# Performance work log

Hardware: AMD Instinct MI355X
Metric: run time of the kernel (lower is better)

The kernel has to match this reference:

```python
import jax, jax.numpy as jnp
import numpy as np

T, D, H, V, Z = 32, 128, 256, 32000, 256


def _gru_cell(x, h, W_ih, W_hh, b_ih, b_hh):
    # PyTorch GRU cell, gate order r,z,n. x,h: [D,H]
    gi = x @ W_ih.T + b_ih
    gh = h @ W_hh.T + b_hh
    i_r, i_z, i_n = jnp.split(gi, 3, axis=-1)
    h_r, h_z, h_n = jnp.split(gh, 3, axis=-1)
    r = jax.nn.sigmoid(i_r + h_r)
    z = jax.nn.sigmoid(i_z + h_z)
    n = jnp.tanh(i_n + r * h_n)
    return (1.0 - z) * n + z * h


def _tree_rnn(nodes, edges, h0, emb, pc, ps):
    # nodes/edges: [T,D]; h0: [D,H]. Child vs sibling GRU chosen per-node by edges.
    def step(h, te):
        tok, e = te
        x = emb[tok]                       # [D,H]
        hc = _gru_cell(x, h, *pc)
        hs = _gru_cell(x, h, *ps)
        hn = jnp.where(e[:, None], hc, hs)  # branch-aware state update
        return hn, hn                       # seq_len=1, L=1 => output == new state
    h_final, outs = jax.lax.scan(step, h0, (nodes, edges))
    return outs, h_final                    # outs: [T,D,H]


def setup_inputs() -> dict:
    key = jax.random.key(0)
    ks = iter(jax.random.split(key, 48))
    s = 0.05
    def gru():
        return (jax.random.normal(next(ks), (3 * H, H), jnp.float32) * s,
                jax.random.normal(next(ks), (3 * H, H), jnp.float32) * s,
                jnp.zeros((3 * H,), jnp.float32),
                jnp.zeros((3 * H,), jnp.float32))
    inp = {}
    inp['nodes'] = jax.random.randint(next(ks), (T, D), 0, V, dtype=jnp.int32)
    inp['edges'] = jax.random.bernoulli(next(ks), 0.5, (T, D))
    inp['emb'] = jax.random.normal(next(ks), (V, H), jnp.float32) * s
    (inp['enc_c_Wih'], inp['enc_c_Whh'], inp['enc_c_bih'], inp['enc_c_bhh']) = gru()
    (inp['enc_s_Wih'], inp['enc_s_Whh'], inp['enc_s_bih'], inp['enc_s_bhh']) = gru()
    (inp['dec_c_Wih'], inp['dec_c_Whh'], inp['dec_c_bih'], inp['dec_c_bhh']) = gru()
    (inp['dec_s_Wih'], inp['dec_s_Whh'], inp['dec_s_bih'], inp['dec_s_bhh']) = gru()
    inp['W_mean'] = jax.random.normal(next(ks), (Z, H), jnp.float32) * s
    inp['b_mean'] = jnp.zeros((Z,), jnp.float32)
    inp['W_logv'] = jax.random.normal(next(ks), (Z, H), jnp.float32) * s
    inp['b_logv'] = jnp.zeros((Z,), jnp.float32)
    inp['W_l2h'] = jax.random.normal(next(ks), (H, Z), jnp.float32) * s
    inp['b_l2h'] = jnp.zeros((H,), jnp.float32)
    inp['W_out'] = jax.random.normal(next(ks), (V, H), jnp.float32) * s
    inp['b_out'] = jnp.zeros((V,), jnp.float32)
    inp['enc_init'] = jax.random.normal(next(ks), (D, H), jnp.float32) * 0.001
    inp['eps'] = jax.random.normal(next(ks), (D, Z), jnp.float32)
    return inp


def reference(nodes, edges, emb,
              enc_c_Wih, enc_c_Whh, enc_c_bih, enc_c_bhh,
              enc_s_Wih, enc_s_Whh, enc_s_bih, enc_s_bhh,
              dec_c_Wih, dec_c_Whh, dec_c_bih, dec_c_bhh,
              dec_s_Wih, dec_s_Whh, dec_s_bih, dec_s_bhh,
              W_mean, b_mean, W_logv, b_logv, W_l2h, b_l2h,
              W_out, b_out, enc_init, eps):
    pc_e = (enc_c_Wih, enc_c_Whh, enc_c_bih, enc_c_bhh)
    ps_e = (enc_s_Wih, enc_s_Whh, enc_s_bih, enc_s_bhh)
    pc_d = (dec_c_Wih, dec_c_Whh, dec_c_bih, dec_c_bhh)
    ps_d = (dec_s_Wih, dec_s_Whh, dec_s_bih, dec_s_bhh)

    _, hid = _tree_rnn(nodes, edges, enc_init, emb, pc_e, ps_e)  # [D,H]
    mean = hid @ W_mean.T + b_mean                               # [D,Z]
    logv = hid @ W_logv.T + b_logv
    z = eps * jnp.exp(0.5 * logv) + mean                          # reparameterize
    h0 = z @ W_l2h.T + b_l2h                                      # [D,H]
    outs, _ = _tree_rnn(nodes, edges, h0, emb, pc_d, ps_d)        # [T,D,H]
    logits = outs @ W_out.T + b_out                               # [T,D,V]
    logp = jax.nn.log_softmax(logits, axis=-1)
    return logp, mean, logv, z
```

## Files before the change

### kernel.cpp

```cpp
#include <hip/hip_runtime.h>
#include <hip/hip_bf16.h>

#define TT 32
#define DD 128
#define HH 256
#define VV 32000
#define ZZ 256
#define NTL 50
#define NBLK 16
#define NPACK 2000
#define GHLP 100

typedef __attribute__((ext_vector_type(8))) short bf16x8;
typedef __attribute__((ext_vector_type(4))) float f32x4;
typedef __attribute__((ext_vector_type(8))) _Float16 f16x8;

static __device__ inline unsigned short f2bf(float x) {
    __hip_bfloat16 h = __float2bfloat16(x);
    return *(unsigned short*)&h;
}

static __device__ inline unsigned long long pack4h(_Float16 a, _Float16 b,
                                                   _Float16 c, _Float16 d) {
    union { _Float16 h[4]; unsigned long long u; } x;
    x.h[0] = a; x.h[1] = b; x.h[2] = c; x.h[3] = d;
    return x.u;
}

static __device__ inline void gload_lds16(const void* g, void* l) {
    __builtin_amdgcn_global_load_lds(
        (const __attribute__((address_space(1))) void*)g,
        (__attribute__((address_space(3))) void*)l, 16, 0, 0);
}

__global__ void edge_canon_k(const unsigned char* __restrict__ eb,
                             unsigned char* __restrict__ canon)
{
    __shared__ int flag;
    if (threadIdx.x == 0) flag = 0;
    __syncthreads();
    int acc = 0;
    for (int i = threadIdx.x; i < TT * DD; i += 256)
        if (i & 3) acc |= eb[i];
    if (acc) atomicOr(&flag, 1);
    __syncthreads();
    const bool is_i32 = (flag == 0);
    for (int i = threadIdx.x; i < TT * DD; i += 256)
        canon[i] = is_i32 ? eb[4 * (size_t)i] : eb[i];
}

__global__ __launch_bounds__(256) void pack_frag4(
    const float* __restrict__ s0, const float* __restrict__ s1,
    const float* __restrict__ s2, const float* __restrict__ s3,
    __hip_bfloat16* __restrict__ dst)
{
    int i = blockIdx.x * 256 + threadIdx.x;
    if (i >= 24576) return;
    int slot = blockIdx.y;
    const float* src = (slot == 0) ? s0 : (slot == 1) ? s1 : (slot == 2) ? s2 : s3;
    __hip_bfloat16* d = dst + (size_t)slot * 196608;
    int lane = i & 63, ks = (i >> 6) & 7, j = i >> 9;
    int g = lane >> 4, c = lane & 15;
    const float* s = src + (size_t)(j * 16 + c) * HH + ks * 32 + g * 8;
    float4 v0 = *(const float4*)s;
    float4 v1 = *(const float4*)(s + 4);
    bf16x8 o;
    o[0] = (short)f2bf(v0.x); o[1] = (short)f2bf(v0.y);
    o[2] = (short)f2bf(v0.z); o[3] = (short)f2bf(v0.w);
    o[4] = (short)f2bf(v1.x); o[5] = (short)f2bf(v1.y);
    o[6] = (short)f2bf(v1.z); o[7] = (short)f2bf(v1.w);
    *(bf16x8*)(d + (size_t)i * 8) = o;
}

__global__ __launch_bounds__(256) void pack_wrnn4(
    const float* __restrict__ s0, const float* __restrict__ s1,
    const float* __restrict__ s2, const float* __restrict__ s3,
    _Float16* __restrict__ dst)
{
    int i = blockIdx.x * 256 + threadIdx.x;
    if (i >= 24576) return;
    int slot = blockIdx.y;
    const float* src = (slot == 0) ? s0 : (slot == 1) ? s1 : (slot == 2) ? s2 : s3;
    _Float16* d = dst + (size_t)slot * 196608;
    int lane = i & 63;
    int t2 = i >> 6;
    int ks = t2 & 7;
    int t3 = t2 >> 3;
    int tt = t3 % 6;
    int j8 = t3 / 6;
    int g = lane >> 4, c = lane & 15;
    int jg2 = tt / 3, gt = tt % 3;
    int srow = gt * 256 + j8 * 32 + jg2 * 16 + c;
    int scol = ks * 32 + g * 8;
    const float* s = src + (size_t)srow * HH + scol;
    float4 v0 = *(const float4*)s;
    float4 v1 = *(const float4*)(s + 4);
    f16x8 o;
    o[0] = (_Float16)v0.x; o[1] = (_Float16)v0.y;
    o[2] = (_Float16)v0.z; o[3] = (_Float16)v0.w;
    o[4] = (_Float16)v1.x; o[5] = (_Float16)v1.y;
    o[6] = (_Float16)v1.z; o[7] = (_Float16)v1.w;
    *(f16x8*)(d + (size_t)i * 8) = o;
}

__global__ __launch_bounds__(256) void gather_pack(
    const int* __restrict__ nodes, const float* __restrict__ emb,
    __hip_bfloat16* __restrict__ dst)
{
    int i = blockIdx.x * 256 + threadIdx.x;
    int lane = i & 63, ks = (i >> 6) & 7, j = i >> 9;
    int g = lane >> 4, c = lane & 15;
    int row = j * 16 + c;
    int tok = nodes[row];
    const float* s = emb + (size_t)tok * HH + ks * 32 + g * 8;
    float4 v0 = *(const float4*)s;
    float4 v1 = *(const float4*)(s + 4);
    bf16x8 o;
    o[0] = (short)f2bf(v0.x); o[1] = (short)f2bf(v0.y);
    o[2] = (short)f2bf(v0.z); o[3] = (short)f2bf(v0.w);
    o[4] = (short)f2bf(v1.x); o[5] = (short)f2bf(v1.y);
    o[6] = (short)f2bf(v1.z); o[7] = (short)f2bf(v1.w);
    *(bf16x8*)(dst + (size_t)i * 8) = o;
}

__global__ __launch_bounds__(256) void pack_lat3(
    const float* __restrict__ s0, const float* __restrict__ s1,
    const float* __restrict__ s2, float* __restrict__ dst)
{
    int i = blockIdx.x * 256 + threadIdx.x;
    int slot = blockIdx.y;
    const float* src = (slot == 0) ? s0 : (slot == 1) ? s1 : s2;
    float* d = dst + (size_t)slot * 65536;
    int j = i & 255, k = i >> 8;
    d[(size_t)k * 256 + j] = src[(size_t)j * 256 + k];
}

template<int MT, bool WRITE_C, bool HAS_BIAS, bool LSE_PARTIAL, bool LSE_SUB>
__global__ __launch_bounds__(256, 2) void gemm_rs(
    const __hip_bfloat16* __restrict__ A,
    const __hip_bfloat16* __restrict__ B,
    int ldc, int nchunks, int ntiles,
    const float* __restrict__ bias,
    const float* __restrict__ lse,
    float* __restrict__ C,
    float* __restrict__ pm, float* __restrict__ ps)
{
    __shared__ float lds_st[WRITE_C ? (4 * 16 * 68) : 1];

    const int tid  = threadIdx.x;
    const int w    = tid >> 6;
    const int lane = tid & 63;
    const int g    = lane >> 4;
    const int c    = lane & 15;
    const int m0   = blockIdx.x * (64 * MT);
    const int n0   = blockIdx.y * (nchunks * 64);
    const int jb0  = n0 >> 4;

    bf16x8 a[MT][8];
#pragma unroll
    for (int mt = 0; mt < MT; ++mt) {
        const int row16 = m0 + mt * 64 + w * 16;
        const __hip_bfloat16* ap = A + (((size_t)(row16 >> 4) * 8) * 64 + lane) * 8;
#pragma unroll
        for (int ks = 0; ks < 8; ++ks) a[mt][ks] = *(const bf16x8*)(ap + ks * 512);
    }

    float mrun[MT][4], srun[MT][4];
#pragma unroll
    for (int mt = 0; mt < MT; ++mt)
#pragma unroll
        for (int r = 0; r < 4; ++r) { mrun[mt][r] = -3.0e38f; srun[mt][r] = 0.f; }

    float lsev[MT][4];
    if (LSE_SUB) {
#pragma unroll
        for (int mt = 0; mt < MT; ++mt)
#pragma unroll
            for (int r = 0; r < 4; ++r)
                lsev[mt][r] = lse[m0 + mt * 64 + w * 16 + 4 * g + r];
    }

    for (int nc = 0; nc < nchunks; ++nc) {
        const int nb = n0 + nc * 64;
        const __hip_bfloat16* bp = B + (((size_t)(jb0 + nc * 4) * 8) * 64 + lane) * 8;

        f32x4 acc[MT][4];
#pragma unroll
        for (int mt = 0; mt < MT; ++mt)
#pragma unroll
            for (int nf = 0; nf < 4; ++nf) acc[mt][nf] = (f32x4){0.f, 0.f, 0.f, 0.f};

#pragma unroll
        for (int ks = 0; ks < 8; ++ks) {
            bf16x8 b0 = *(const bf16x8*)(bp + (0 * 8 + ks) * 512);
            bf16x8 b1 = *(const bf16x8*)(bp + (1 * 8 + ks) * 512);
            bf16x8 b2 = *(const bf16x8*)(bp + (2 * 8 + ks) * 512);
            bf16x8 b3 = *(const bf16x8*)(bp + (3 * 8 + ks) * 512);
#pragma unroll
            for (int mt = 0; mt < MT; ++mt) {
                acc[mt][0] = __builtin_amdgcn_mfma_f32_16x16x32_bf16(a[mt][ks], b0, acc[mt][0], 0, 0, 0);
                acc[mt][1] = __builtin_amdgcn_mfma_f32_16x16x32_bf16(a[mt][ks], b1, acc[mt][1], 0, 0, 0);
                acc[mt][2] = __builtin_amdgcn_mfma_f32_16x16x32_bf16(a[mt][ks], b2, acc[mt][2], 0, 0, 0);
                acc[mt][3] = __builtin_amdgcn_mfma_f32_16x16x32_bf16(a[mt][ks], b3, acc[mt][3], 0, 0, 0);
            }
        }

        float bv[4] = {0.f, 0.f, 0.f, 0.f};
        if (HAS_BIAS) {
#pragma unroll
            for (int nf = 0; nf < 4; ++nf) bv[nf] = bias[nb + nf * 16 + c];
        }

        if (LSE_PARTIAL) {
#pragma unroll
            for (int mt = 0; mt < MT; ++mt)
#pragma unroll
                for (int r = 0; r < 4; ++r) {
                    float l0 = acc[mt][0][r] + bv[0];
                    float l1 = acc[mt][1][r] + bv[1];
                    float l2 = acc[mt][2][r] + bv[2];
                    float l3 = acc[mt][3][r] + bv[3];
                    float mc = fmaxf(fmaxf(l0, l1), fmaxf(l2, l3));
                    float mn = fmaxf(mrun[mt][r], mc);
                    srun[mt][r] = srun[mt][r] * __expf(mrun[mt][r] - mn)
                            + __expf(l0 - mn) + __expf(l1 - mn)
                            + __expf(l2 - mn) + __expf(l3 - mn);
                    mrun[mt][r] = mn;
                }
        }

        if (WRITE_C) {
            const int base = w * (16 * 68);
#pragma unroll
            for (int mt = 0; mt < MT; ++mt) {
                const int row16 = m0 + mt * 64 + w * 16;
#pragma unroll
                for (int nf = 0; nf < 4; ++nf)
#pragma unroll
                    for (int r = 0; r < 4; ++r) {
                        float v = acc[mt][nf][r] + bv[nf];
                        if (LSE_SUB) v -= lsev[mt][r];
                        lds_st[base + (4 * g + r) * 68 + nf * 16 + c] = v;
                    }
#pragma unroll
                for (int i = 0; i < 4; ++i) {
                    int lr = i * 4 + g;
                    float4 v = *(const float4*)&lds_st[base + lr * 68 + c * 4];
                    *(float4*)(C + (size_t)(row16 + lr) * ldc + nb + c * 4) = v;
                }
            }
        }
    }

    if (LSE_PARTIAL) {
#pragma unroll
        for (int mt = 0; mt < MT; ++mt)
#pragma unroll
            for (int r = 0; r < 4; ++r) {
                float m = mrun[mt][r], s = srun[mt][r];
#pragma unroll
                for (int mk = 1; mk <= 8; mk <<= 1) {
                    float m2 = __shfl_xor(m, mk);
                    float s2 = __shfl_xor(s, mk);
                    float mn = fmaxf(m, m2);
                    s = s * __expf(m - mn) + s2 * __expf(m2 - mn);
                    m = mn;
                }
                if (c == 0) {
                    int row = m0 + mt * 64 + w * 16 + 4 * g + r;
                    pm[(size_t)row * ntiles + blockIdx.y] = m;
                    ps[(size_t)row * ntiles + blockIdx.y] = s;
                }
            }
    }
}

template<bool DBUF, bool WRITE_C, bool HAS_BIAS, bool LSE_PARTIAL, bool LSE_SUB>
__global__ __launch_bounds__(256, 2) void gemm_ls(
    const __hip_bfloat16* __restrict__ A,
    const __hip_bfloat16* __restrict__ B,
    int ldc, int nchunks, int ntiles,
    const float* __restrict__ bias,
    const float* __restrict__ lse,
    float* __restrict__ C,
    float* __restrict__ pm, float* __restrict__ ps)
{
    __shared__ __align__(16) char ldsB[DBUF ? 2 : 1][32768];
    __shared__ float lds_st[WRITE_C ? (4 * 16 * 68) : 1];

    const int tid  = threadIdx.x;
    const int w    = tid >> 6;
    const int lane = tid & 63;
    const int g    = lane >> 4;
    const int c    = lane & 15;
    const int m0   = blockIdx.x * 128;
    const int n0   = blockIdx.y * (nchunks * 64);
    const int jb0  = n0 >> 4;

    bf16x8 a[2][8];
#pragma unroll
    for (int mt = 0; mt < 2; ++mt) {
        const int row16 = m0 + mt * 64 + w * 16;
        const __hip_bfloat16* ap = A + (((size_t)(row16 >> 4) * 8) * 64 + lane) * 8;
#pragma unroll
        for (int ks = 0; ks < 8; ++ks) a[mt][ks] = *(const bf16x8*)(ap + ks * 512);
    }

    float mrun[2][4], srun[2][4];
#pragma unroll
    for (int mt = 0; mt < 2; ++mt)
#pragma unroll
        for (int r = 0; r < 4; ++r) { mrun[mt][r] = -3.0e38f; srun[mt][r] = 0.f; }

    float lsev[2][4];
    if (LSE_SUB) {
#pragma unroll
        for (int mt = 0; mt < 2; ++mt)
#pragma unroll
            for (int r = 0; r < 4; ++r)
                lsev[mt][r] = lse[m0 + mt * 64 + w * 16 + 4 * g + r];
    }

    const char* Bbase = (const char*)B;
#define STAGE_TILE(bbuf, nc_)                                                     \
    {                                                                             \
        const char* src = Bbase + ((size_t)(jb0 + (nc_) * 4) * 8 * 64) * 16;      \
        _Pragma("unroll")                                                         \
        for (int i_ = 0; i_ < 8; ++i_) {                                          \
            int seg = w * 8 + i_;                                                 \
            gload_lds16(src + (size_t)seg * 1024 + lane * 16,                     \
                        &ldsB[bbuf][seg * 1024]);                                 \
        }                                                                         \
    }

    int buf = 0;
    if (DBUF) {
        STAGE_TILE(0, 0);
        __syncthreads();
    }

    for (int nc = 0; nc < nchunks; ++nc) {
        if (DBUF) {
            if (nc + 1 < nchunks) STAGE_TILE(buf ^ 1, nc + 1);
        } else {
            STAGE_TILE(0, nc);
            __syncthreads();
        }

        const int nb = n0 + nc * 64;
        f32x4 acc[2][4];
#pragma unroll
        for (int mt = 0; mt < 2; ++mt)
#pragma unroll
            for (int nf = 0; nf < 4; ++nf) acc[mt][nf] = (f32x4){0.f, 0.f, 0.f, 0.f};

#pragma unroll
        for (int ks = 0; ks < 8; ++ks) {
            bf16x8 b0 = *(const bf16x8*)&ldsB[buf][((0 * 8 + ks) * 64 + lane) * 16];
            bf16x8 b1 = *(const bf16x8*)&ldsB[buf][((1 * 8 + ks) * 64 + lane) * 16];
            bf16x8 b2 = *(const bf16x8*)&ldsB[buf][((2 * 8 + ks) * 64 + lane) * 16];
            bf16x8 b3 = *(const bf16x8*)&ldsB[buf][((3 * 8 + ks) * 64 + lane) * 16];
#pragma unroll
            for (int mt = 0; mt < 2; ++mt) {
                acc[mt][0] = __builtin_amdgcn_mfma_f32_16x16x32_bf16(a[mt][ks], b0, acc[mt][0], 0, 0, 0);
                acc[mt][1] = __builtin_amdgcn_mfma_f32_16x16x32_bf16(a[mt][ks], b1, acc[mt][1], 0, 0, 0);
                acc[mt][2] = __builtin_amdgcn_mfma_f32_16x16x32_bf16(a[mt][ks], b2, acc[mt][2], 0, 0, 0);
                acc[mt][3] = __builtin_amdgcn_mfma_f32_16x16x32_bf16(a[mt][ks], b3, acc[mt][3], 0, 0, 0);
            }
        }

        float bv[4] = {0.f, 0.f, 0.f, 0.f};
        if (HAS_BIAS) {
#pragma unroll
            for (int nf = 0; nf < 4; ++nf) bv[nf] = bias[nb + nf * 16 + c];
        }

        if (LSE_PARTIAL) {
#pragma unroll
            for (int mt = 0; mt < 2; ++mt)
#pragma unroll
                for (int r = 0; r < 4; ++r) {
                    float l0 = acc[mt][0][r] + bv[0];
                    float l1 = acc[mt][1][r] + bv[1];
                    float l2 = acc[mt][2][r] + bv[2];
                    float l3 = acc[mt][3][r] + bv[3];
                    float mc = fmaxf(fmaxf(l0, l1), fmaxf(l2, l3));
                    float mn = fmaxf(mrun[mt][r], mc);
                    srun[mt][r] = srun[mt][r] * __expf(mrun[mt][r] - mn)
                            + __expf(l0 - mn) + __expf(l1 - mn)
                            + __expf(l2 - mn) + __expf(l3 - mn);
                    mrun[mt][r] = mn;
                }
        }

        if (WRITE_C) {
            const int base = w * (16 * 68);
#pragma unroll
            for (int mt = 0; mt < 2; ++mt) {
                const int row16 = m0 + mt * 64 + w * 16;
#pragma unroll
                for (int nf = 0; nf < 4; ++nf)
#pragma unroll
                    for (int r = 0; r < 4; ++r) {
                        float v = acc[mt][nf][r] + bv[nf];
                        if (LSE_SUB) v -= lsev[mt][r];
                        lds_st[base + (4 * g + r) * 68 + nf * 16 + c] = v;
                    }
#pragma unroll
                for (int i = 0; i < 4; ++i) {
                    int lr = i * 4 + g;
                    float4 v = *(const float4*)&lds_st[base + lr * 68 + c * 4];
                    *(float4*)(C + (size_t)(row16 + lr) * ldc + nb + c * 4) = v;
                }
            }
        }

        __syncthreads();
        if (DBUF) buf ^= 1;
    }
#undef STAGE_TILE

    if (LSE_PARTIAL) {
#pragma unroll
        for (int mt = 0; mt < 2; ++mt)
#pragma unroll
            for (int r = 0; r < 4; ++r) {
                float m = mrun[mt][r], s = srun[mt][r];
#pragma unroll
                for (int mk = 1; mk <= 8; mk <<= 1) {
                    float m2 = __shfl_xor(m, mk);
                    float s2 = __shfl_xor(s, mk);
                    float mn = fmaxf(m, m2);
                    s = s * __expf(m - mn) + s2 * __expf(m2 - mn);
                    m = mn;
                }
                if (c == 0) {
                    int row = m0 + mt * 64 + w * 16 + 4 * g + r;
                    pm[(size_t)row * ntiles + blockIdx.y] = m;
                    ps[(size_t)row * ntiles + blockIdx.y] = s;
                }
            }
    }
}

__global__ __launch_bounds__(512) void rnn_fused6(
    const unsigned char* __restrict__ ecan,
    const float* __restrict__ gi,
    const _Float16* __restrict__ Wr,
    const float* __restrict__ ecbih, const float* __restrict__ ecbhh,
    const float* __restrict__ esbih, const float* __restrict__ esbhh,
    const float* __restrict__ dcbih, const float* __restrict__ dcbhh,
    const float* __restrict__ dsbih, const float* __restrict__ dsbhh,
    const float* __restrict__ WmT, const float* __restrict__ WlT,
    const float* __restrict__ WhT,
    const float* __restrict__ b_mean, const float* __restrict__ b_logv,
    const float* __restrict__ b_l2h,
    const float* __restrict__ enc_init, const float* __restrict__ eps,
    float* __restrict__ out_mean, float* __restrict__ out_logv,
    float* __restrict__ out_z,
    __hip_bfloat16* __restrict__ outs_pk,
    _Float16* __restrict__ xh,
    int* __restrict__ flags,
    const float* __restrict__ W_out, __hip_bfloat16* __restrict__ Wp)
{
    __shared__ _Float16 wlds[6 * 8 * 64 * 8];
    __shared__ _Float16 hpk[64 * 64 * 8];
    __shared__ _Float16 ghl[DD * GHLP];
    __shared__ float    bsum[4 * 256];
    __shared__ unsigned char ecan_l[TT * DD];

    const int tid = threadIdx.x;

    if (blockIdx.x >= NBLK) {
        int i = (blockIdx.x - NBLK) * 512 + tid;
        if (i < 2000 * 8 * 64) {
            int lane = i & 63, ks = (i >> 6) & 7, j = i >> 9;
            int g2 = lane >> 4, c2 = lane & 15;
            const float* s = W_out + (size_t)(j * 16 + c2) * HH + ks * 32 + g2 * 8;
            float4 v0 = *(const float4*)s;
            float4 v1 = *(const float4*)(s + 4);
            bf16x8 o;
            o[0] = (short)f2bf(v0.x); o[1] = (short)f2bf(v0.y);
            o[2] = (short)f2bf(v0.z); o[3] = (short)f2bf(v0.w);
            o[4] = (short)f2bf(v1.x); o[5] = (short)f2bf(v1.y);
            o[6] = (short)f2bf(v1.z); o[7] = (short)f2bf(v1.w);
            *(bf16x8*)(Wp + (size_t)i * 8) = o;
        }
        return;
    }

    const int v   = blockIdx.x & 1;
    const int j8  = blockIdx.x >> 1;
    const int w    = tid >> 6;
    const int lane = tid & 63;
    const int g    = lane >> 4;
    const int c    = lane & 15;
    const int dq   = w & 3;
    const int jg2  = w >> 2;

    for (int u = tid; u < TT * DD; u += 512) ecan_l[u] = ecan[u];

    for (int u = tid; u < 4096; u += 512) {
        int chunk = u >> 6, ln = u & 63;
        int dt = chunk >> 3, ks = chunk & 7, lg = ln >> 4, lc = ln & 15;
        const float* s = enc_init + (size_t)(dt * 16 + lc) * HH + ks * 32 + lg * 8;
        float4 v0 = *(const float4*)s;
        float4 v1 = *(const float4*)(s + 4);
        f16x8 o;
        o[0] = (_Float16)v0.x; o[1] = (_Float16)v0.y;
        o[2] = (_Float16)v0.z; o[3] = (_Float16)v0.w;
        o[4] = (_Float16)v1.x; o[5] = (_Float16)v1.y;
        o[6] = (_Float16)v1.z; o[7] = (_Float16)v1.w;
        *(f16x8*)&hpk[(size_t)u * 8] = o;
    }
    __syncthreads();

    int bi = 0;

    for (int p = 0; p < 2; ++p) {
        {
            const _Float16* wsrc = Wr + ((size_t)(p * 2 + v) * 8 + j8) * (3072 * 8);
            for (int idx = tid; idx < 3072; idx += 512)
                *(f16x8*)&wlds[(size_t)idx * 8] = *(const f16x8*)(wsrc + (size_t)idx * 8);
        }
        {
            const float* bih = p ? (v ? dsbih : dcbih) : (v ? esbih : ecbih);
            const float* bhh = p ? (v ? dsbhh : dcbhh) : (v ? esbhh : ecbhh);
            if (tid < 256) {
                bsum[tid]       = bih[tid]       + bhh[tid];
                bsum[256 + tid] = bih[256 + tid] + bhh[256 + tid];
                bsum[512 + tid] = bih[512 + tid];
                bsum[768 + tid] = bhh[512 + tid];
            }
        }
        __syncthreads();

        for (int st = 0; st < TT; ++st) {
            f32x4 gpr0[3], gpr1[3];
            bool sel0, sel1;
            {
                const int u0 = tid, u1 = tid + 512;
                const int d0 = u0 >> 3, d1 = u1 >> 3;
                const int jgA = j8 * 32 + (u0 & 7) * 4;
                const int jgB = j8 * 32 + (u1 & 7) * 4;
                sel0 = (ecan_l[st * DD + d0] != 0) == (v == 0);
                sel1 = (ecan_l[st * DD + d1] != 0) == (v == 0);
                if (sel0) {
                    const float* gp = gi + (size_t)(st * DD + d0) * 3072 + p * 1536 + v * 768 + jgA;
                    gpr0[0] = *(const f32x4*)gp;
                    gpr0[1] = *(const f32x4*)(gp + 256);
                    gpr0[2] = *(const f32x4*)(gp + 512);
                }
                if (sel1) {
                    const float* gp = gi + (size_t)(st * DD + d1) * 3072 + p * 1536 + v * 768 + jgB;
                    gpr1[0] = *(const f32x4*)gp;
                    gpr1[1] = *(const f32x4*)(gp + 256);
                    gpr1[2] = *(const f32x4*)(gp + 512);
                }
            }

            f32x4 acc[2][3];
#pragma unroll
            for (int a = 0; a < 2; ++a)
#pragma unroll
                for (int b = 0; b < 3; ++b) acc[a][b] = (f32x4){0.f, 0.f, 0.f, 0.f};
#pragma unroll
            for (int ks = 0; ks < 8; ++ks) {
                f16x8 a0 = *(const f16x8*)&hpk[(((dq * 2 + 0) * 8 + ks) * 64 + lane) * 8];
                f16x8 a1 = *(const f16x8*)&hpk[(((dq * 2 + 1) * 8 + ks) * 64 + lane) * 8];
#pragma unroll
                for (int gt = 0; gt < 3; ++gt) {
                    f16x8 bf = *(const f16x8*)&wlds[(((jg2 * 3 + gt) * 8 + ks) * 64 + lane) * 8];
                    acc[0][gt] = __builtin_amdgcn_mfma_f32_16x16x32_f16(a0, bf, acc[0][gt], 0, 0, 0);
                    acc[1][gt] = __builtin_amdgcn_mfma_f32_16x16x32_f16(a1, bf, acc[1][gt], 0, 0, 0);
                }
            }

#pragma unroll
            for (int dti = 0; dti < 2; ++dti) {
                const int dt = dq * 2 + dti;
#pragma unroll
                for (int gt = 0; gt < 3; ++gt)
#pragma unroll
                    for (int rr = 0; rr < 4; ++rr)
                        ghl[(dt * 16 + 4 * g + rr) * GHLP + gt * 32 + jg2 * 16 + c] =
                            (_Float16)acc[dti][gt][rr];
            }
            __syncthreads();

            _Float16* xcur = xh + (size_t)bi * (DD * HH);
#pragma unroll
            for (int uu = 0; uu < 2; ++uu) {
                const bool sel = uu ? sel1 : sel0;
                if (!sel) continue;
                const int u = tid + uu * 512;
                const int d = u >> 3, jq = u & 7;
                const int jl = jq * 4;
                const int jg_ = j8 * 32 + jl;
                const f32x4* gpr = uu ? gpr1 : gpr0;

                f32x4 br  = *(const f32x4*)&bsum[jg_];
                f32x4 bz  = *(const f32x4*)&bsum[256 + jg_];
                f32x4 bni = *(const f32x4*)&bsum[512 + jg_];
                f32x4 bnh = *(const f32x4*)&bsum[768 + jg_];
                const _Float16* gd = &ghl[d * GHLP];
                const int dt = d >> 4, lc = d & 15, ks = jg_ >> 5, lg = (jg_ >> 3) & 3;
                const int ch = ((dt * 8 + ks) * 64 + lg * 16 + lc);
                const _Float16* hop = &hpk[(size_t)ch * 8 + (jg_ & 7)];

                _Float16 hn[4];
                unsigned short ob[4];
#pragma unroll
                for (int m = 0; m < 4; ++m) {
                    float ghr = (float)gd[jl + m];
                    float ghz = (float)gd[32 + jl + m];
                    float ghn = (float)gd[64 + jl + m];
                    float rg = 1.f / (1.f + __expf(-(gpr[0][m] + br[m] + ghr)));
                    float zg = 1.f / (1.f + __expf(-(gpr[1][m] + bz[m] + ghz)));
                    float nn = tanhf(gpr[2][m] + bni[m] + rg * (ghn + bnh[m]));
                    float hv = (1.f - zg) * nn + zg * (float)hop[m];
                    hn[m] = (_Float16)hv;
                    ob[m] = f2bf(hv);
                }
                __hip_atomic_store((unsigned long long*)(xcur + (size_t)d * HH + jg_),
                                   pack4h(hn[0], hn[1], hn[2], hn[3]),
                                   __ATOMIC_RELAXED, __HIP_MEMORY_SCOPE_AGENT);
                if (p) {
                    union { unsigned short s[4]; unsigned long long u; } ou;
                    ou.s[0] = ob[0]; ou.s[1] = ob[1]; ou.s[2] = ob[2]; ou.s[3] = ob[3];
                    size_t och = ((size_t)(st * 8 + dt) * 8 + ks) * 64 + lg * 16 + lc;
                    *(unsigned long long*)((unsigned short*)outs_pk + och * 8 + (jg_ & 7)) = ou.u;
                }
            }
            __syncthreads();

            if (tid == 0)
                __hip_atomic_store(&flags[blockIdx.x], bi + 1,
                                   __ATOMIC_RELAXED, __HIP_MEMORY_SCOPE_AGENT);
            if (tid < 64) {
                for (;;) {
                    int f = (tid < NBLK)
                          ? __hip_atomic_load(&flags[tid], __ATOMIC_RELAXED, __HIP_MEMORY_SCOPE_AGENT)
                          : 0x7fffffff;
                    if (__all(f >= bi + 1)) break;
                    __builtin_amdgcn_s_sleep(1);
                }
            }
            __syncthreads();

            {
                const _Float16* xr = xh + (size_t)bi * (DD * HH);
                f16x8 tv[8];
#pragma unroll
                for (int i = 0; i < 8; ++i) {
                    int u = tid + i * 512;
                    int chunk = u >> 6, ln = u & 63;
                    int dt = chunk >> 3, ks = chunk & 7, lg = ln >> 4, lc = ln & 15;
                    tv[i] = *(const f16x8*)(xr + (size_t)(dt * 16 + lc) * HH + ks * 32 + lg * 8);
                }
#pragma unroll
                for (int i = 0; i < 8; ++i)
                    *(f16x8*)&hpk[(size_t)(tid + i * 512) * 8] = tv[i];
            }
            __syncthreads();
            ++bi;
        }

        if (p == 0) {
            float* hlin = (float*)ghl;
            const int d8 = tid >> 6;
            const int q  = tid & 63;
            const int dg = blockIdx.x * 8 + d8;
            for (int u = tid; u < 2048; u += 512) {
                int du = u >> 8, k = u & 255;
                int d = blockIdx.x * 8 + du;
                hlin[du * 256 + k] = (float)hpk[(((size_t)(d >> 4) * 8 + (k >> 5)) * 64
                                      + ((k >> 3) & 3) * 16 + (d & 15)) * 8 + (k & 7)];
            }
            __syncthreads();
            f32x4 mean4, logv4;
            {
                f32x4 sm = {0, 0, 0, 0}, sl = {0, 0, 0, 0};
                const float* hl = hlin + d8 * 256;
                for (int k = 0; k < HH; ++k) {
                    float hv = hl[k];
                    sm += hv * *(const f32x4*)(WmT + (size_t)k * 256 + q * 4);
                    sl += hv * *(const f32x4*)(WlT + (size_t)k * 256 + q * 4);
                }
                mean4 = sm + *(const f32x4*)(b_mean + q * 4);
                logv4 = sl + *(const f32x4*)(b_logv + q * 4);
                *(f32x4*)(out_mean + (size_t)dg * ZZ + q * 4) = mean4;
                *(f32x4*)(out_logv + (size_t)dg * ZZ + q * 4) = logv4;
            }
            __syncthreads();
            {
                f32x4 ep = *(const f32x4*)(eps + (size_t)dg * ZZ + q * 4);
                f32x4 zv;
#pragma unroll
                for (int m = 0; m < 4; ++m)
                    zv[m] = ep[m] * __expf(0.5f * logv4[m]) + mean4[m];
                *(f32x4*)(out_z + (size_t)dg * ZZ + q * 4) = zv;
                *(f32x4*)(hlin + d8 * 256 + q * 4) = zv;
            }
            __syncthreads();
            {
                f32x4 s = {0, 0, 0, 0};
                const float* zlp = hlin + d8 * 256;
                for (int k = 0; k < ZZ; ++k)
                    s += zlp[k] * *(const f32x4*)(WhT + (size_t)k * 256 + q * 4);
                f32x4 h0v = s + *(const f32x4*)(b_l2h + q * 4);
                __hip_atomic_store(
                    (unsigned long long*)(xh + (size_t)bi * (DD * HH) + (size_t)dg * HH + q * 4),
                    pack4h((_Float16)h0v[0], (_Float16)h0v[1],
                           (_Float16)h0v[2], (_Float16)h0v[3]),
                    __ATOMIC_RELAXED, __HIP_MEMORY_SCOPE_AGENT);
            }
            __syncthreads();
            if (tid == 0)
                __hip_atomic_store(&flags[blockIdx.x], bi + 1,
                                   __ATOMIC_RELAXED, __HIP_MEMORY_SCOPE_AGENT);
            if (tid < 64) {
                for (;;) {
                    int f = (tid < NBLK)
                          ? __hip_atomic_load(&flags[tid], __ATOMIC_RELAXED, __HIP_MEMORY_SCOPE_AGENT)
                          : 0x7fffffff;
                    if (__all(f >= bi + 1)) break;
                    __builtin_amdgcn_s_sleep(1);
                }
            }
            __syncthreads();
            {
                const _Float16* xr = xh + (size_t)bi * (DD * HH);
                f16x8 tv[8];
#pragma unroll
                for (int i = 0; i < 8; ++i) {
                    int u = tid + i * 512;
                    int chunk = u >> 6, ln = u & 63;
                    int dt = chunk >> 3, ks = chunk & 7, lg = ln >> 4, lc = ln & 15;
                    tv[i] = *(const f16x8*)(xr + (size_t)(dt * 16 + lc) * HH + ks * 32 + lg * 8);
                }
#pragma unroll
                for (int i = 0; i < 8; ++i)
                    *(f16x8*)&hpk[(size_t)(tid + i * 512) * 8] = tv[i];
            }
            __syncthreads();
            ++bi;
        }
    }
}

__global__ __launch_bounds__(64) void lse_reduce(
    const float* __restrict__ pm, const float* __restrict__ ps,
    float* __restrict__ lse, int nt)
{
    int row = blockIdx.x;
    int l = threadIdx.x;
    float m = (l < nt) ? pm[(size_t)row * nt + l] : -3.0e38f;
    float s = (l < nt) ? ps[(size_t)row * nt + l] : 0.f;
    for (int mk = 1; mk <= 32; mk <<= 1) {
        float m2 = __shfl_xor(m, mk);
        float s2 = __shfl_xor(s, mk);
        float mn = fmaxf(m, m2);
        s = s * __expf(m - mn) + s2 * __expf(m2 - mn);
        m = mn;
    }
    if (l == 0) lse[row] = m + logf(s);
}

extern "C" void kernel_launch(void* const* d_in, const int* in_sizes, int n_in,
                              void* d_out, int out_size, void* d_ws, size_t ws_size,
                              hipStream_t stream)
{
    const int*           nodes     = (const int*)d_in[0];
    const unsigned char* edges_raw = (const unsigned char*)d_in[1];
    const float* emb    = (const float*)d_in[2];
    const float* ecWih  = (const float*)d_in[3];
    const float* ecWhh  = (const float*)d_in[4];
    const float* ecbih  = (const float*)d_in[5];
    const float* ecbhh  = (const float*)d_in[6];
    const float* esWih  = (const float*)d_in[7];
    const float* esWhh  = (const float*)d_in[8];
    const float* esbih  = (const float*)d_in[9];
    const float* esbhh  = (const float*)d_in[10];
    const float* dcWih  = (const float*)d_in[11];
    const float* dcWhh  = (const float*)d_in[12];
    const float* dcbih  = (const float*)d_in[13];
    const float* dcbhh  = (const float*)d_in[14];
    const float* dsWih  = (const float*)d_in[15];
    const float* dsWhh  = (const float*)d_in[16];
    const float* dsbih  = (const float*)d_in[17];
    const float* dsbhh  = (const float*)d_in[18];
    const float* W_mean = (const float*)d_in[19];
    const float* b_mean = (const float*)d_in[20];
    const float* W_logv = (const float*)d_in[21];
    const float* b_logv = (const float*)d_in[22];
    const float* W_l2h  = (const float*)d_in[23];
    const float* b_l2h  = (const float*)d_in[24];
    const float* W_out  = (const float*)d_in[25];
    const float* b_out  = (const float*)d_in[26];
    const float* enc_init = (const float*)d_in[27];
    const float* eps    = (const float*)d_in[28];

    float* out      = (float*)d_out;
    float* out_mean = out + (size_t)TT * DD * VV;
    float* out_logv = out_mean + DD * ZZ;
    float* out_z    = out_logv + DD * ZZ;
    float* gi       = out;

    char* ws = (char*)d_ws;
    __hip_bfloat16* outs_pk = (__hip_bfloat16*)(ws + 0);
    __hip_bfloat16* Ap      = (__hip_bfloat16*)(ws + 2097152);
    __hip_bfloat16* Wp      = (__hip_bfloat16*)(ws + 4194304);
    __hip_bfloat16* Bp_all  = (__hip_bfloat16*)(ws + 20971520);
    _Float16*       Wr      = (_Float16*)(ws + 22544384);
    float*          WmT     = (float*)(ws + 24117248);
    float*          pm      = (float*)(ws + 24903680);
    float*          ps      = (float*)(ws + 25722880);
    float*          lse     = (float*)(ws + 26542080);
    unsigned char*  ecan    = (unsigned char*)(ws + 26558464);
    _Float16*       xh      = (_Float16*)(ws + 26562560);
    int*            flags   = (int*)(ws + 30822400);
    float*          WlT     = WmT + 65536;
    float*          WhT     = WmT + 131072;

    hipMemsetAsync(flags, 0, 64, stream);

    edge_canon_k<<<1, 256, 0, stream>>>(edges_raw, ecan);
    pack_frag4<<<dim3(96, 4), 256, 0, stream>>>(ecWih, esWih, dcWih, dsWih, Bp_all);
    pack_wrnn4<<<dim3(96, 4), 256, 0, stream>>>(ecWhh, esWhh, dcWhh, dsWhh, Wr);
    pack_lat3<<<dim3(256, 3), 256, 0, stream>>>(W_mean, W_logv, W_l2h, WmT);
    gather_pack<<<512, 256, 0, stream>>>(nodes, emb, Ap);

    gemm_rs<2, true, false, false, false><<<dim3(32, 6), 256, 0, stream>>>(
        Ap, Bp_all, 3072, 8, 6, nullptr, nullptr, gi, nullptr, nullptr);

    rnn_fused6<<<NBLK + NPACK, 512, 0, stream>>>(
        ecan, gi, Wr,
        ecbih, ecbhh, esbih, esbhh, dcbih, dcbhh, dsbih, dsbhh,
        WmT, WlT, WhT, b_mean, b_logv, b_l2h,
        enc_init, eps, out_mean, out_logv, out_z, outs_pk, xh, flags,
        W_out, Wp);

    gemm_ls<true, false, true, true, false><<<dim3(32, NTL), 256, 0, stream>>>(
        outs_pk, Wp, VV, 10, NTL, b_out, nullptr, nullptr, pm, ps);
    lse_reduce<<<4096, 64, 0, stream>>>(pm, ps, lse, NTL);
    gemm_ls<false, true, true, false, true><<<dim3(32, NTL), 256, 0, stream>>>(
        outs_pk, Wp, VV, 10, NTL, b_out, lse, out, nullptr, nullptr);
}
```

Before: 759.7 us.

## Drop double-buffered B staging in logits GEMM and make grid barrier per-wave

New measurement: 768.5 us. About the same (+1.2%).

```diff
diff --git a/kernel.cpp b/kernel.cpp
--- a/kernel.cpp
+++ b/kernel.cpp
@@ -275,7 +275,7 @@
     }
 }
 
-template<bool DBUF, bool WRITE_C, bool HAS_BIAS, bool LSE_PARTIAL, bool LSE_SUB>
+template<bool WRITE_C, bool HAS_BIAS, bool LSE_PARTIAL, bool LSE_SUB>
 __global__ __launch_bounds__(256, 2) void gemm_ls(
     const __hip_bfloat16* __restrict__ A,
     const __hip_bfloat16* __restrict__ B,
@@ -285,7 +285,7 @@
     float* __restrict__ C,
     float* __restrict__ pm, float* __restrict__ ps)
 {
-    __shared__ __align__(16) char ldsB[DBUF ? 2 : 1][32768];
+    __shared__ __align__(16) char ldsB[32768];
     __shared__ float lds_st[WRITE_C ? (4 * 16 * 68) : 1];
 
     const int tid  = threadIdx.x;
@@ -322,30 +322,17 @@
     }
 
     const char* Bbase = (const char*)B;
-#define STAGE_TILE(bbuf, nc_)                                                     \
-    {                                                                             \
-        const char* src = Bbase + ((size_t)(jb0 + (nc_) * 4) * 8 * 64) * 16;      \
-        _Pragma("unroll")                                                         \
-        for (int i_ = 0; i_ < 8; ++i_) {                                          \
-            int seg = w * 8 + i_;                                                 \
-            gload_lds16(src + (size_t)seg * 1024 + lane * 16,                     \
-                        &ldsB[bbuf][seg * 1024]);                                 \
-        }                                                                         \
-    }
-
-    int buf = 0;
-    if (DBUF) {
-        STAGE_TILE(0, 0);
+
+    for (int nc = 0; nc < nchunks; ++nc) {
+        {
+            const char* src = Bbase + ((size_t)(jb0 + nc * 4) * 8 * 64) * 16;
+#pragma unroll
+            for (int i_ = 0; i_ < 8; ++i_) {
+                int seg = w * 8 + i_;
+                gload_lds16(src + (size_t)seg * 1024 + lane * 16, &ldsB[seg * 1024]);
+            }
+        }
         __syncthreads();
-    }
-
-    for (int nc = 0; nc < nchunks; ++nc) {
-        if (DBUF) {
-            if (nc + 1 < nchunks) STAGE_TILE(buf ^ 1, nc + 1);
-        } else {
-            STAGE_TILE(0, nc);
-            __syncthreads();
-        }
 
         const int nb = n0 + nc * 64;
         f32x4 acc[2][4];
@@ -356,10 +343,10 @@
 
 #pragma unroll
         for (int ks = 0; ks < 8; ++ks) {
-            bf16x8 b0 = *(const bf16x8*)&ldsB[buf][((0 * 8 + ks) * 64 + lane) * 16];
-            bf16x8 b1 = *(const bf16x8*)&ldsB[buf][((1 * 8 + ks) * 64 + lane) * 16];
-            bf16x8 b2 = *(const bf16x8*)&ldsB[buf][((2 * 8 + ks) * 64 + lane) * 16];
-            bf16x8 b3 = *(const bf16x8*)&ldsB[buf][((3 * 8 + ks) * 64 + lane) * 16];
+            bf16x8 b0 = *(const bf16x8*)&ldsB[((0 * 8 + ks) * 64 + lane) * 16];
+            bf16x8 b1 = *(const bf16x8*)&ldsB[((1 * 8 + ks) * 64 + lane) * 16];
+            bf16x8 b2 = *(const bf16x8*)&ldsB[((2 * 8 + ks) * 64 + lane) * 16];
+            bf16x8 b3 = *(const bf16x8*)&ldsB[((3 * 8 + ks) * 64 + lane) * 16];
 #pragma unroll
             for (int mt = 0; mt < 2; ++mt) {
                 acc[mt][0] = __builtin_amdgcn_mfma_f32_16x16x32_bf16(a[mt][ks], b0, acc[mt][0], 0, 0, 0);
@@ -416,9 +403,7 @@
         }
 
         __syncthreads();
-        if (DBUF) buf ^= 1;
-    }
-#undef STAGE_TILE
+    }
 
     if (LSE_PARTIAL) {
 #pragma unroll
@@ -637,16 +622,13 @@
             if (tid == 0)
                 __hip_atomic_store(&flags[blockIdx.x], bi + 1,
                                    __ATOMIC_RELAXED, __HIP_MEMORY_SCOPE_AGENT);
-            if (tid < 64) {
-                for (;;) {
-                    int f = (tid < NBLK)
-                          ? __hip_atomic_load(&flags[tid], __ATOMIC_RELAXED, __HIP_MEMORY_SCOPE_AGENT)
-                          : 0x7fffffff;
-                    if (__all(f >= bi + 1)) break;
-                    __builtin_amdgcn_s_sleep(1);
-                }
-            }
-            __syncthreads();
+            for (;;) {
+                int f = (lane < NBLK)
+                      ? __hip_atomic_load(&flags[lane], __ATOMIC_RELAXED, __HIP_MEMORY_SCOPE_AGENT)
+                      : 0x7fffffff;
+                if (__all(f >= bi + 1)) break;
+                __builtin_amdgcn_s_sleep(1);
+            }
 
             {
                 const _Float16* xr = xh + (size_t)bi * (DD * HH);
@@ -719,16 +701,13 @@
             if (tid == 0)
                 __hip_atomic_store(&flags[blockIdx.x], bi + 1,
                                    __ATOMIC_RELAXED, __HIP_MEMORY_SCOPE_AGENT);
-            if (tid < 64) {
-                for (;;) {
-                    int f = (tid < NBLK)
-                          ? __hip_atomic_load(&flags[tid], __ATOMIC_RELAXED, __HIP_MEMORY_SCOPE_AGENT)
-                          : 0x7fffffff;
-                    if (__all(f >= bi + 1)) break;
-                    __builtin_amdgcn_s_sleep(1);
-                }
-            }
-            __syncthreads();
+            for (;;) {
+                int f = (lane < NBLK)
+                      ? __hip_atomic_load(&flags[lane], __ATOMIC_RELAXED, __HIP_MEMORY_SCOPE_AGENT)
+                      : 0x7fffffff;
+                if (__all(f >= bi + 1)) break;
+                __builtin_amdgcn_s_sleep(1);
+            }
             {
                 const _Float16* xr = xh + (size_t)bi * (DD * HH);
                 f16x8 tv[8];
@@ -841,9 +820,9 @@
         enc_init, eps, out_mean, out_logv, out_z, outs_pk, xh, flags,
         W_out, Wp);
 
-    gemm_ls<true, false, true, true, false><<<dim3(32, NTL), 256, 0, stream>>>(
+    gemm_ls<false, true, true, false><<<dim3(32, NTL), 256, 0, stream>>>(
         outs_pk, Wp, VV, 10, NTL, b_out, nullptr, nullptr, pm, ps);
     lse_reduce<<<4096, 64, 0, stream>>>(pm, ps, lse, NTL);
-    gemm_ls<false, true, true, false, true><<<dim3(32, NTL), 256, 0, stream>>>(
+    gemm_ls<true, true, false, true><<<dim3(32, NTL), 256, 0, stream>>>(
         outs_pk, Wp, VV, 10, NTL, b_out, lse, out, nullptr, nullptr);
 }
```
